# Kernel tuning notes

Hardware: AMD Instinct MI355X
Metric: run time of the kernel (lower is better)

Reference implementation:

```python
import jax, jax.numpy as jnp
import numpy as np


def setup_inputs() -> dict:
    key = jax.random.key(0)
    k1, k2 = jax.random.split(key)
    x = jax.random.normal(k1, (8192, 128), dtype=jnp.float32)
    y = jax.random.normal(k2, (8192, 128), dtype=jnp.float32)
    return {"x": x, "y": y}


def reference(x, y):
    # Squared pairwise euclidean distances: ||x_i||^2 + ||y_j||^2 - 2 x_i . y_j
    num_pts = x.shape[0]
    x2 = jnp.sum(x * x, axis=1)  # [N]
    y2 = jnp.sum(y * y, axis=1)  # [M]
    dist = x2[:, None] + y2[None, :] - 2.0 * (x @ y.T)  # [N, M]
    dist = jnp.maximum(dist, 0.0)  # matches pow(cdist, 2) up to fp rounding
    in_dist_out = jnp.min(dist, axis=0)   # per-y nearest x, [M]
    out_dist_in = jnp.min(dist, axis=1)   # per-x nearest y, [N]
    loss = jnp.sum(in_dist_out + out_dist_in) / num_pts
    return loss
```

## Files before the change

kernel.cpp:

```cpp
#include <hip/hip_runtime.h>
#include <hip/hip_bf16.h>
#include <stdint.h>


typedef __bf16  bf16x8 __attribute__((ext_vector_type(8)));
typedef float   f32x4  __attribute__((ext_vector_type(4)));

#define NPTS 8192
#define DIM  128
#define KC   128

__device__ __forceinline__ void gload_lds16(const void* gsrc, void* ldst) {
  __builtin_amdgcn_global_load_lds(
      (const __attribute__((address_space(1))) uint32_t*)(uintptr_t)gsrc,
      (__attribute__((address_space(3))) uint32_t*)(uintptr_t)ldst,
      16, 0, 0);
}

__global__ __launch_bounds__(256) void prep_kernel(
    const float* __restrict__ x, const float* __restrict__ y,
    unsigned short* __restrict__ Xc, unsigned short* __restrict__ Yc,
    float* __restrict__ x2, float* __restrict__ y2,
    unsigned int* __restrict__ minx, unsigned int* __restrict__ miny)
{
  const int gt  = blockIdx.x * 256 + threadIdx.x;
  const int row = gt >> 5;
  const int seg = gt & 31;
  const bool isx = row < NPTS;
  const float* src        = isx ? (x  + (size_t)row * DIM) : (y  + (size_t)(row - NPTS) * DIM);
  unsigned short* dst     = isx ? (Xc + (size_t)row * KC)  : (Yc + (size_t)(row - NPTS) * KC);

  f32x4 v = *reinterpret_cast<const f32x4*>(src + seg * 4);
  float sq = v[0]*v[0] + v[1]*v[1] + v[2]*v[2] + v[3]*v[3];
  #pragma unroll
  for (int m = 1; m <= 16; m <<= 1) sq += __shfl_xor(sq, m);
  if (seg == 0) { if (isx) x2[row] = sq; else y2[row - NPTS] = sq; }

  const float scale = isx ? -2.0f : 1.0f;
  unsigned short hb[4];
  #pragma unroll
  for (int i = 0; i < 4; ++i) {
    __hip_bfloat16 h = __float2bfloat16(scale * v[i]);
    hb[i] = __builtin_bit_cast(unsigned short, h);
  }
  *reinterpret_cast<ushort4*>(dst + seg * 4) = make_ushort4(hb[0], hb[1], hb[2], hb[3]);

  if (gt < NPTS)          minx[gt]        = 0x7F800000u;
  else if (gt < 2 * NPTS) miny[gt - NPTS] = 0x7F800000u;
}

__global__ __launch_bounds__(512, 2) void chamfer_gemm(
    const unsigned short* __restrict__ Xc, const unsigned short* __restrict__ Yc,
    const float* __restrict__ x2, const float* __restrict__ y2,
    unsigned int* __restrict__ minx, unsigned int* __restrict__ miny)
{
  __shared__ alignas(16) unsigned short As[2][256 * 64];
  __shared__ alignas(16) unsigned short Bs[2][256 * 64];
  __shared__ float colminLDS[2 * 256];
  __shared__ float rowminLDS[4 * 256];

  const int tid  = threadIdx.x;
  const int lane = tid & 63;
  const int w    = tid >> 6;
  const int wr   = w >> 2;
  const int wc   = w & 3;

  const int b     = blockIdx.x;
  const int local = b >> 3;
  const int bi    = (b & 7) * 4 + (local >> 3);
  const int bj0   = (local & 7) * 4;

  const int r64  = tid >> 3;
  const int kgrp = (tid & 7) ^ (r64 & 7);
  const unsigned short* Abase = Xc + (size_t)(bi * 256 + r64) * KC + kgrp * 8;
  const int wofs = w * 1024;

  auto STAGE_A = [&](int kt) {
    const unsigned short* Asrc = Abase + kt * 64;
    char* Ad = (char*)&As[kt][0] + wofs;
    #pragma unroll
    for (int l = 0; l < 4; ++l)
      gload_lds16(Asrc + (size_t)l * 64 * KC, Ad + l * 8192);
  };
  auto STAGE_B = [&](int buf, int t, int kt) {
    const unsigned short* Bsrc = Yc + (size_t)((bj0 + t) * 256 + r64) * KC + kgrp * 8 + kt * 64;
    char* Bd = (char*)&Bs[buf][0] + wofs;
    #pragma unroll
    for (int l = 0; l < 4; ++l)
      gload_lds16(Bsrc + (size_t)l * 64 * KC, Bd + l * 8192);
  };

  STAGE_A(0);
  STAGE_A(1);
  STAGE_B(0, 0, 0);

  f32x4 xv[8];
  #pragma unroll
  for (int mi = 0; mi < 8; ++mi)
    xv[mi] = *reinterpret_cast<const f32x4*>(x2 + bi * 256 + wr * 128 + mi * 16 + ((lane >> 4) << 2));
  float yv[4];
  #pragma unroll
  for (int ni = 0; ni < 4; ++ni)
    yv[ni] = y2[bj0 * 256 + wc * 64 + ni * 16 + (lane & 15)];

  float rowrun0 = 3.0e38f, rowrun1 = 3.0e38f;

  __syncthreads();

  for (int t = 0; t < 4; ++t) {
    f32x4 acc[8][4];
    #pragma unroll
    for (int mi = 0; mi < 8; ++mi)
      #pragma unroll
      for (int ni = 0; ni < 4; ++ni)
        #pragma unroll
        for (int r = 0; r < 4; ++r)
          acc[mi][ni][r] = xv[mi][r] + yv[ni];

    float yvn[4];
    if (t < 3) {
      #pragma unroll
      for (int ni = 0; ni < 4; ++ni)
        yvn[ni] = y2[(bj0 + t + 1) * 256 + wc * 64 + ni * 16 + (lane & 15)];
    }

    #pragma unroll
    for (int kt = 0; kt < 2; ++kt) {
      if (kt == 0)      STAGE_B(1, t, 1);
      else if (t < 3)   STAGE_B(0, t + 1, 0);

      const char* Ab = (const char*)&As[kt][0];
      const char* Bb = (const char*)&Bs[kt][0];

      bf16x8 bfr[4][2];
      #pragma unroll
      for (int ni = 0; ni < 4; ++ni) {
        const int col = wc * 64 + ni * 16 + (lane & 15);
        const int swz = (col & 7) << 4;
        #pragma unroll
        for (int ks = 0; ks < 2; ++ks) {
          const int ofs = (ks * 64 + ((lane >> 4) << 4)) ^ swz;
          bfr[ni][ks] = *reinterpret_cast<const bf16x8*>(Bb + col * 128 + ofs);
        }
      }
      #pragma unroll
      for (int mi = 0; mi < 8; ++mi) {
        const int rowl = wr * 128 + mi * 16 + (lane & 15);
        const int swz  = (rowl & 7) << 4;
        const bf16x8 a0 = *reinterpret_cast<const bf16x8*>(Ab + rowl * 128 + ((  0 + ((lane >> 4) << 4)) ^ swz));
        const bf16x8 a1 = *reinterpret_cast<const bf16x8*>(Ab + rowl * 128 + (( 64 + ((lane >> 4) << 4)) ^ swz));
        #pragma unroll
        for (int ni = 0; ni < 4; ++ni) {
          acc[mi][ni] = __builtin_amdgcn_mfma_f32_16x16x32_bf16(a0, bfr[ni][0], acc[mi][ni], 0, 0, 0);
          acc[mi][ni] = __builtin_amdgcn_mfma_f32_16x16x32_bf16(a1, bfr[ni][1], acc[mi][ni], 0, 0, 0);
        }
      }
      __syncthreads();
    }

    float cm[4];
    #pragma unroll
    for (int ni = 0; ni < 4; ++ni) {
      float m = 3.0e38f;
      #pragma unroll
      for (int mi = 0; mi < 8; ++mi)
        #pragma unroll
        for (int r = 0; r < 4; ++r)
          m = fminf(m, acc[mi][ni][r]);
      cm[ni] = m;
    }
    {
      const bool hb0 = (lane & 16) != 0;
      float s0 = hb0 ? cm[0] : cm[2];
      float s1 = hb0 ? cm[1] : cm[3];
      float r0 = __shfl_xor(s0, 16);
      float r1 = __shfl_xor(s1, 16);
      float t0 = fminf(hb0 ? cm[2] : cm[0], r0);
      float t1 = fminf(hb0 ? cm[3] : cm[1], r1);
      const bool hb1 = (lane & 32) != 0;
      float s  = hb1 ? t0 : t1;
      float rr = __shfl_xor(s, 32);
      float cfin = fminf(hb1 ? t1 : t0, rr);
      const int ni = (hb0 ? 2 : 0) + (hb1 ? 1 : 0);
      colminLDS[wr * 256 + wc * 64 + ni * 16 + (lane & 15)] = cfin;
    }

    float rm[32];
    #pragma unroll
    for (int mi = 0; mi < 8; ++mi)
      #pragma unroll
      for (int r = 0; r < 4; ++r)
        rm[mi * 4 + r] = fminf(fminf(acc[mi][0][r], acc[mi][1][r]),
                               fminf(acc[mi][2][r], acc[mi][3][r]));
    #pragma unroll
    for (int b2 = 0; b2 < 4; ++b2) {
      const int  half = 16 >> b2;
      const bool up   = (lane >> b2) & 1;
      #pragma unroll
      for (int i = 0; i < half; ++i) {
        float snd = up ? rm[i] : rm[i + half];
        float rcv = __shfl_xor(snd, 1 << b2);
        rm[i] = fminf(up ? rm[i + half] : rm[i], rcv);
      }
    }
    {
      const int base = ((lane & 1) << 4) | ((lane & 2) << 2) | (lane & 4) | ((lane & 8) >> 2);
      #pragma unroll
      for (int e = 0; e < 2; ++e) {
        const int idx = base | e;
        const int row_local = wr * 128 + (idx >> 2) * 16 + ((lane >> 4) << 2) + (idx & 3);
        rowminLDS[wc * 256 + row_local] = rm[e];
      }
    }
    __syncthreads();

    if (tid < 256) {
      float c = fminf(colminLDS[tid], colminLDS[256 + tid]);
      atomicMin(&miny[(bj0 + t) * 256 + tid], __float_as_uint(fmaxf(c, 0.f)));
    } else {
      const int r = tid - 256;
      float v = fminf(fminf(rowminLDS[r], rowminLDS[256 + r]),
                      fminf(rowminLDS[512 + r], rowminLDS[768 + r]));
      rowrun0 = fminf(rowrun0, v);
    }
    (void)rowrun1;

    #pragma unroll
    for (int ni = 0; ni < 4; ++ni) yv[ni] = yvn[ni];
  }

  if (tid >= 256)
    atomicMin(&minx[bi * 256 + (tid - 256)], __float_as_uint(fmaxf(rowrun0, 0.f)));
}

__global__ __launch_bounds__(256) void finalize_kernel(
    const unsigned int* __restrict__ minx, const unsigned int* __restrict__ miny,
    float* __restrict__ out)
{
  const f32x4* mx = (const f32x4*)minx;
  const f32x4* my = (const f32x4*)miny;
  float s = 0.f;
  for (int i = threadIdx.x; i < NPTS / 4; i += 256) {
    f32x4 a = mx[i], b = my[i];
    s += (a[0] + a[1] + a[2] + a[3]) + (b[0] + b[1] + b[2] + b[3]);
  }
  #pragma unroll
  for (int m = 32; m >= 1; m >>= 1) s += __shfl_xor(s, m);
  __shared__ float partial[4];
  if ((threadIdx.x & 63) == 0) partial[threadIdx.x >> 6] = s;
  __syncthreads();
  if (threadIdx.x == 0)
    out[0] = (partial[0] + partial[1] + partial[2] + partial[3]) * (1.0f / (float)NPTS);
}

extern "C" void kernel_launch(void* const* d_in, const int* in_sizes, int n_in,
                              void* d_out, int out_size, void* d_ws, size_t ws_size,
                              hipStream_t stream) {
  (void)in_sizes; (void)n_in; (void)out_size; (void)ws_size;
  const float* x = (const float*)d_in[0];
  const float* y = (const float*)d_in[1];
  char* ws = (char*)d_ws;

  unsigned short* Xc  = (unsigned short*)(ws);
  unsigned short* Yc  = (unsigned short*)(ws + 2097152);
  float*          x2  = (float*)(ws + 4194304);
  float*          y2  = (float*)(ws + 4227072);
  unsigned int*   mnx = (unsigned int*)(ws + 4259840);
  unsigned int*   mny = (unsigned int*)(ws + 4292608);
  float*          out = (float*)d_out;

  prep_kernel<<<2048, 256, 0, stream>>>(x, y, Xc, Yc, x2, y2, mnx, mny);
  chamfer_gemm<<<256, 512, 0, stream>>>(Xc, Yc, x2, y2, mnx, mny);
  finalize_kernel<<<1, 256, 0, stream>>>(mnx, mny, out);
}
```

Before: 86.05 us.

## Load B fragments directly from global into registers and drop LDS reductions

```diff
diff --git a/kernel.cpp b/kernel.cpp
--- a/kernel.cpp
+++ b/kernel.cpp
@@ -55,9 +55,6 @@
     unsigned int* __restrict__ minx, unsigned int* __restrict__ miny)
 {
   __shared__ alignas(16) unsigned short As[2][256 * 64];
-  __shared__ alignas(16) unsigned short Bs[2][256 * 64];
-  __shared__ float colminLDS[2 * 256];
-  __shared__ float rowminLDS[4 * 256];
 
   const int tid  = threadIdx.x;
   const int lane = tid & 63;
@@ -75,74 +72,68 @@
   const unsigned short* Abase = Xc + (size_t)(bi * 256 + r64) * KC + kgrp * 8;
   const int wofs = w * 1024;
 
-  auto STAGE_A = [&](int kt) {
+  #pragma unroll
+  for (int kt = 0; kt < 2; ++kt) {
     const unsigned short* Asrc = Abase + kt * 64;
     char* Ad = (char*)&As[kt][0] + wofs;
     #pragma unroll
     for (int l = 0; l < 4; ++l)
       gload_lds16(Asrc + (size_t)l * 64 * KC, Ad + l * 8192);
-  };
-  auto STAGE_B = [&](int buf, int t, int kt) {
-    const unsigned short* Bsrc = Yc + (size_t)((bj0 + t) * 256 + r64) * KC + kgrp * 8 + kt * 64;
-    char* Bd = (char*)&Bs[buf][0] + wofs;
-    #pragma unroll
-    for (int l = 0; l < 4; ++l)
-      gload_lds16(Bsrc + (size_t)l * 64 * KC, Bd + l * 8192);
-  };
-
-  STAGE_A(0);
-  STAGE_A(1);
-  STAGE_B(0, 0, 0);
-
-  f32x4 xv[8];
-  #pragma unroll
-  for (int mi = 0; mi < 8; ++mi)
-    xv[mi] = *reinterpret_cast<const f32x4*>(x2 + bi * 256 + wr * 128 + mi * 16 + ((lane >> 4) << 2));
-  float yv[4];
+  }
+
+  __syncthreads();
+
+  const unsigned short* Bf[4];
   #pragma unroll
   for (int ni = 0; ni < 4; ++ni)
-    yv[ni] = y2[bj0 * 256 + wc * 64 + ni * 16 + (lane & 15)];
+    Bf[ni] = Yc + (size_t)(wc * 64 + ni * 16 + (lane & 15)) * KC + (lane >> 4) * 8;
+
+  int4 bq[2][4][2];
+  #pragma unroll
+  for (int ni = 0; ni < 4; ++ni)
+    #pragma unroll
+    for (int ks = 0; ks < 2; ++ks)
+      bq[0][ni][ks] = *reinterpret_cast<const int4*>(Bf[ni] + (size_t)bj0 * 256 * KC + ks * 32);
 
   float rowrun0 = 3.0e38f, rowrun1 = 3.0e38f;
 
-  __syncthreads();
-
+  #pragma unroll
   for (int t = 0; t < 4; ++t) {
+    const int bj = bj0 + t;
+
     f32x4 acc[8][4];
-    #pragma unroll
-    for (int mi = 0; mi < 8; ++mi)
+    {
+      f32x4 xv; float yv[4];
       #pragma unroll
       for (int ni = 0; ni < 4; ++ni)
-        #pragma unroll
-        for (int r = 0; r < 4; ++r)
-          acc[mi][ni][r] = xv[mi][r] + yv[ni];
-
-    float yvn[4];
-    if (t < 3) {
-      #pragma unroll
-      for (int ni = 0; ni < 4; ++ni)
-        yvn[ni] = y2[(bj0 + t + 1) * 256 + wc * 64 + ni * 16 + (lane & 15)];
+        yv[ni] = y2[bj * 256 + wc * 64 + ni * 16 + (lane & 15)];
+      #pragma unroll
+      for (int mi = 0; mi < 8; ++mi) {
+        xv = *reinterpret_cast<const f32x4*>(x2 + bi * 256 + wr * 128 + mi * 16 + ((lane >> 4) << 2));
+        #pragma unroll
+        for (int ni = 0; ni < 4; ++ni)
+          #pragma unroll
+          for (int r = 0; r < 4; ++r)
+            acc[mi][ni][r] = xv[r] + yv[ni];
+      }
     }
 
     #pragma unroll
     for (int kt = 0; kt < 2; ++kt) {
-      if (kt == 0)      STAGE_B(1, t, 1);
-      else if (t < 3)   STAGE_B(0, t + 1, 0);
+      const int p = (t * 2 + kt) & 1;
+
+      if (t * 2 + kt < 7) {
+        const int nt  = (kt == 1) ? t + 1 : t;
+        const int nkt = kt ^ 1;
+        #pragma unroll
+        for (int ni = 0; ni < 4; ++ni)
+          #pragma unroll
+          for (int ks = 0; ks < 2; ++ks)
+            bq[p ^ 1][ni][ks] = *reinterpret_cast<const int4*>(
+                Bf[ni] + (size_t)(bj0 + nt) * 256 * KC + nkt * 64 + ks * 32);
+      }
 
       const char* Ab = (const char*)&As[kt][0];
-      const char* Bb = (const char*)&Bs[kt][0];
-
-      bf16x8 bfr[4][2];
-      #pragma unroll
-      for (int ni = 0; ni < 4; ++ni) {
-        const int col = wc * 64 + ni * 16 + (lane & 15);
-        const int swz = (col & 7) << 4;
-        #pragma unroll
-        for (int ks = 0; ks < 2; ++ks) {
-          const int ofs = (ks * 64 + ((lane >> 4) << 4)) ^ swz;
-          bfr[ni][ks] = *reinterpret_cast<const bf16x8*>(Bb + col * 128 + ofs);
-        }
-      }
       #pragma unroll
       for (int mi = 0; mi < 8; ++mi) {
         const int rowl = wr * 128 + mi * 16 + (lane & 15);
@@ -151,11 +142,12 @@
         const bf16x8 a1 = *reinterpret_cast<const bf16x8*>(Ab + rowl * 128 + (( 64 + ((lane >> 4) << 4)) ^ swz));
         #pragma unroll
         for (int ni = 0; ni < 4; ++ni) {
-          acc[mi][ni] = __builtin_amdgcn_mfma_f32_16x16x32_bf16(a0, bfr[ni][0], acc[mi][ni], 0, 0, 0);
-          acc[mi][ni] = __builtin_amdgcn_mfma_f32_16x16x32_bf16(a1, bfr[ni][1], acc[mi][ni], 0, 0, 0);
+          acc[mi][ni] = __builtin_amdgcn_mfma_f32_16x16x32_bf16(
+              a0, __builtin_bit_cast(bf16x8, bq[p][ni][0]), acc[mi][ni], 0, 0, 0);
+          acc[mi][ni] = __builtin_amdgcn_mfma_f32_16x16x32_bf16(
+              a1, __builtin_bit_cast(bf16x8, bq[p][ni][1]), acc[mi][ni], 0, 0, 0);
         }
       }
-      __syncthreads();
     }
 
     float cm[4];
@@ -182,7 +174,8 @@
       float rr = __shfl_xor(s, 32);
       float cfin = fminf(hb1 ? t1 : t0, rr);
       const int ni = (hb0 ? 2 : 0) + (hb1 ? 1 : 0);
-      colminLDS[wr * 256 + wc * 64 + ni * 16 + (lane & 15)] = cfin;
+      atomicMin(&miny[bj * 256 + wc * 64 + ni * 16 + (lane & 15)],
+                __float_as_uint(fmaxf(cfin, 0.f)));
     }
 
     float rm[32];
@@ -203,34 +196,19 @@
         rm[i] = fminf(up ? rm[i + half] : rm[i], rcv);
       }
     }
-    {
-      const int base = ((lane & 1) << 4) | ((lane & 2) << 2) | (lane & 4) | ((lane & 8) >> 2);
-      #pragma unroll
-      for (int e = 0; e < 2; ++e) {
-        const int idx = base | e;
-        const int row_local = wr * 128 + (idx >> 2) * 16 + ((lane >> 4) << 2) + (idx & 3);
-        rowminLDS[wc * 256 + row_local] = rm[e];
-      }
-    }
-    __syncthreads();
-
-    if (tid < 256) {
-      float c = fminf(colminLDS[tid], colminLDS[256 + tid]);
-      atomicMin(&miny[(bj0 + t) * 256 + tid], __float_as_uint(fmaxf(c, 0.f)));
-    } else {
-      const int r = tid - 256;
-      float v = fminf(fminf(rowminLDS[r], rowminLDS[256 + r]),
-                      fminf(rowminLDS[512 + r], rowminLDS[768 + r]));
-      rowrun0 = fminf(rowrun0, v);
-    }
-    (void)rowrun1;
-
-    #pragma unroll
-    for (int ni = 0; ni < 4; ++ni) yv[ni] = yvn[ni];
-  }
-
-  if (tid >= 256)
-    atomicMin(&minx[bi * 256 + (tid - 256)], __float_as_uint(fmaxf(rowrun0, 0.f)));
+    rowrun0 = fminf(rowrun0, rm[0]);
+    rowrun1 = fminf(rowrun1, rm[1]);
+  }
+
+  {
+    const int base = ((lane & 1) << 4) | ((lane & 2) << 2) | (lane & 4) | ((lane & 8) >> 2);
+    const int idx0 = base;
+    const int idx1 = base | 1;
+    const int row0 = wr * 128 + (idx0 >> 2) * 16 + ((lane >> 4) << 2) + (idx0 & 3);
+    const int row1 = wr * 128 + (idx1 >> 2) * 16 + ((lane >> 4) << 2) + (idx1 & 3);
+    atomicMin(&minx[bi * 256 + row0], __float_as_uint(fmaxf(rowrun0, 0.f)));
+    atomicMin(&minx[bi * 256 + row1], __float_as_uint(fmaxf(rowrun1, 0.f)));
+  }
 }
 
 __global__ __launch_bounds__(256) void finalize_kernel(
```

New measurement: 107.8 us. +25.2%, slower.
